# Optimization experiments

Measured on AMD Instinct MI355X. Metric: run time of the kernel, lower is better.

## Reference

```python
import jax, jax.numpy as jnp
import numpy as np

B, L, D_IN = 32, 200, 64
H = 64          # hidden_size
A = 36          # attention_size
NEG_SLOPE = 0.01  # torch LeakyReLU default


def setup_inputs() -> dict:
    key = jax.random.key(0)
    ks = jax.random.split(key, 7)
    s_ln = 1.0 / np.sqrt(D_IN)
    s_w1 = 1.0 / np.sqrt(3 * H)
    s_w2 = 1.0 / np.sqrt(A)
    return {
        "x": jax.random.normal(ks[0], (B, L, D_IN), dtype=jnp.float32),
        "ln_w": jax.random.uniform(ks[1], (D_IN, H), minval=-s_ln, maxval=s_ln, dtype=jnp.float32),
        "ln_b": jax.random.uniform(ks[2], (H,), minval=-s_ln, maxval=s_ln, dtype=jnp.float32),
        "w1": jax.random.uniform(ks[3], (3 * H, A), minval=-s_w1, maxval=s_w1, dtype=jnp.float32),
        "b1": jax.random.uniform(ks[4], (A,), minval=-s_w1, maxval=s_w1, dtype=jnp.float32),
        "w2": jax.random.uniform(ks[5], (A,), minval=-s_w2, maxval=s_w2, dtype=jnp.float32),
        "b2": jax.random.uniform(ks[6], (), minval=-s_w2, maxval=s_w2, dtype=jnp.float32),
    }


def reference(x, ln_w, ln_b, w1, b1, w2, b2):
    # x: [B, L, D_in] -> h: [B, L, H]
    h = jnp.einsum("bld,dh->blh", x, ln_w) + ln_b
    Ld = h.shape[1]
    Hd = h.shape[-1]
    # The torch code concatenates (x1, x2, x1*x2) where x1[b,i,j]=h[b,j],
    # x2[b,i,j]=h[b,i]. Split w1 accordingly instead of materializing the
    # [B,L,L,3H] concat tensor.
    w1a, w1b, w1c = w1[:Hd], w1[Hd:2 * Hd], w1[2 * Hd:]
    a = jnp.einsum("bjh,ha->bja", h, w1a)          # x1 contribution (depends on j)
    c = jnp.einsum("bih,ha->bia", h, w1b)          # x2 contribution (depends on i)
    cross = jnp.einsum("bih,bjh,ha->bija", h, h, w1c)  # (x1*x2) contribution
    pre = a[:, None, :, :] + c[:, :, None, :] + cross + b1   # [B,L,L,A]
    act = jax.nn.leaky_relu(pre, negative_slope=NEG_SLOPE)
    score = jnp.einsum("bija,a->bij", act, w2) + b2          # [B,L,L]
    mask = jnp.tril(jnp.ones((Ld, Ld), dtype=score.dtype))   # causal (incl. diag)
    score = score * mask
    return jnp.einsum("bij,bjh->bih", score, h)               # [B,L,H]
```

## Files before the change

kernel.cpp:

```cpp
#include <hip/hip_runtime.h>

#define B 32
#define L 200
#define DIN 64
#define H 64
#define A 36

typedef __attribute__((ext_vector_type(8))) short short8;
typedef __attribute__((ext_vector_type(4))) float floatx4;
typedef __attribute__((ext_vector_type(8))) float floatx8;

static __device__ __forceinline__ short f2bf(float f) {
    union { float f; unsigned u; } v; v.f = f;
    unsigned r = (v.u + 0x7FFF + ((v.u >> 16) & 1)) >> 16;
    return (short)r;
}
static __device__ __forceinline__ float bf2f(short s) {
    union { unsigned u; float f; } v; v.u = ((unsigned)(unsigned short)s) << 16;
    return v.f;
}

__global__ __launch_bounds__(256) void prep_kernel(
    const float* __restrict__ x, const float* __restrict__ ln_w,
    const float* __restrict__ ln_b, const float* __restrict__ w1,
    float* __restrict__ h_out, float* __restrict__ cc_out, short* __restrict__ hb16_out,
    float* __restrict__ w1a_r, float* __restrict__ w1c_r)
{
    int wave = threadIdx.x >> 6;
    int lane = threadIdx.x & 63;
    int bl = __builtin_amdgcn_readfirstlane(blockIdx.x * 4 + wave);
    const float* xr = x + (size_t)bl * DIN;
    float p0 = ln_b[lane], p1 = 0.f;
    #pragma unroll
    for (int d = 0; d < DIN; d += 2) {
        p0 = fmaf(xr[d],     ln_w[d * H + lane],       p0);
        p1 = fmaf(xr[d + 1], ln_w[(d + 1) * H + lane], p1);
    }
    float acc = p0 + p1;
    __shared__ float hrow[4][H];
    hrow[wave][lane] = acc;
    h_out[(size_t)bl * H + lane] = acc;
    int j = bl % L;
    hb16_out[(size_t)bl * H + (lane ^ ((j & 7) << 3))] = f2bf(acc);
    if (lane < A) {
        float s0 = 0.f, s1 = 0.f;
        #pragma unroll
        for (int hh = 0; hh < H; hh += 2) {
            s0 = fmaf(hrow[wave][hh],     w1[(H + hh) * A + lane],     s0);
            s1 = fmaf(hrow[wave][hh + 1], w1[(H + hh + 1) * A + lane], s1);
        }
        cc_out[(size_t)bl * A + lane] = s0 + s1;
    }
    if (blockIdx.x == 0) {
        for (int idx = threadIdx.x; idx < 2 * 3 * 64 * 8; idx += 256) {
            int e = idx & 7, ln = (idx >> 3) & 63, sn = idx >> 9;
            int s = sn / 3, n = sn - 3 * s;
            int k = s * 32 + (ln >> 4) * 8 + e;
            int c = n * 16 + (ln & 15);
            w1a_r[idx] = (c < A) ? w1[k * A + c] : 0.f;
            w1c_r[idx] = (c < A) ? w1[(2 * H + k) * A + c] : 0.f;
        }
    }
}

__global__ __launch_bounds__(256) void score_kernel(
    const float* __restrict__ h, const short* __restrict__ hb16,
    const float* __restrict__ cc, const float* __restrict__ w1a_r,
    const float* __restrict__ w1c_r, const float* __restrict__ b1,
    const float* __restrict__ w2, const float* __restrict__ b2,
    float* __restrict__ out)
{
    int blk = blockIdx.x;
    int b  = blk / 50;
    int bg = blk - b * 50;
    int wave = threadIdx.x >> 6;
    int lane = threadIdx.x & 63;
    int i = __builtin_amdgcn_readfirstlane(bg + 50 * wave);
    int l15 = lane & 15, l4 = lane >> 4;

    __shared__ __align__(16) short tile[208 * 64];
    __shared__ __align__(16) float slds[4][16];

    const short* hb16b = hb16 + (size_t)b * L * H;

    for (int c = wave; c < 26; c += 4) {
        int j = (c < 25) ? (c * 8 + (lane >> 3)) : (L - 1);
        const short* src = hb16b + (size_t)j * H + (lane & 7) * 8;
        __builtin_amdgcn_global_load_lds(
            (const __attribute__((address_space(1))) void*)src,
            (__attribute__((address_space(3))) void*)&tile[c * 512],
            16, 0, 0);
    }

    const float* hi    = h + ((size_t)b * L + i) * H;
    const float* ccrow = cc + ((size_t)b * L + i) * A;
    float b2v = b2[0];
    float w2v[3][4], cbv[3][4];
    #pragma unroll
    for (int n = 0; n < 3; ++n) {
        #pragma unroll
        for (int r = 0; r < 4; ++r) {
            int a = n * 16 + l4 * 4 + r;
            bool av = a < A;
            w2v[n][r] = av ? w2[a] : 0.f;
            cbv[n][r] = av ? (ccrow[a] + b1[a]) : 0.f;
        }
    }
    short8 afrag[2][3];
    #pragma unroll
    for (int s = 0; s < 2; ++s) {
        float hik[8];
        #pragma unroll
        for (int e = 0; e < 8; ++e) hik[e] = hi[s * 32 + l4 * 8 + e];
        #pragma unroll
        for (int n = 0; n < 3; ++n) {
            floatx8 wa = *(const floatx8*)&w1a_r[(((s * 3 + n) * 64) + lane) * 8];
            floatx8 wc = *(const floatx8*)&w1c_r[(((s * 3 + n) * 64) + lane) * 8];
            #pragma unroll
            for (int e = 0; e < 8; ++e)
                afrag[s][n][e] = f2bf(fmaf(hik[e], wc[e], wa[e]));
        }
    }
    __syncthreads();

    float oacc[4] = {0.f, 0.f, 0.f, 0.f};
    int mmax = (i >> 4) + 1;

    for (int m = 0; m < mmax; ++m) {
        int row = m * 16 + l15;
        const short* brow = tile + row * 64;
        int sw = (l15 & 7) << 3;
        short8 bf0 = *(const short8*)(brow + ((l4 * 8) ^ sw));
        short8 bf1 = *(const short8*)(brow + ((32 + l4 * 8) ^ sw));
        floatx4 c0 = {cbv[0][0], cbv[0][1], cbv[0][2], cbv[0][3]};
        floatx4 c1 = {cbv[1][0], cbv[1][1], cbv[1][2], cbv[1][3]};
        floatx4 c2 = {cbv[2][0], cbv[2][1], cbv[2][2], cbv[2][3]};
        c0 = __builtin_amdgcn_mfma_f32_16x16x32_bf16(afrag[0][0], bf0, c0, 0, 0, 0);
        c1 = __builtin_amdgcn_mfma_f32_16x16x32_bf16(afrag[0][1], bf0, c1, 0, 0, 0);
        c2 = __builtin_amdgcn_mfma_f32_16x16x32_bf16(afrag[0][2], bf0, c2, 0, 0, 0);
        c0 = __builtin_amdgcn_mfma_f32_16x16x32_bf16(afrag[1][0], bf1, c0, 0, 0, 0);
        c1 = __builtin_amdgcn_mfma_f32_16x16x32_bf16(afrag[1][1], bf1, c1, 0, 0, 0);
        c2 = __builtin_amdgcn_mfma_f32_16x16x32_bf16(afrag[1][2], bf1, c2, 0, 0, 0);
        float sp = 0.f;
        #pragma unroll
        for (int r = 0; r < 4; ++r) {
            float v0 = c0[r], v1 = c1[r], v2 = c2[r];
            float a0 = fmaf(0.01f, fminf(v0, 0.f), fmaxf(v0, 0.f));
            float a1 = fmaf(0.01f, fminf(v1, 0.f), fmaxf(v1, 0.f));
            float a2 = fmaf(0.01f, fminf(v2, 0.f), fmaxf(v2, 0.f));
            sp = fmaf(a0, w2v[0][r], sp);
            sp = fmaf(a1, w2v[1][r], sp);
            sp = fmaf(a2, w2v[2][r], sp);
        }
        sp += __shfl_xor(sp, 16, 64);
        sp += __shfl_xor(sp, 32, 64);
        float sc = (row <= i) ? sp + b2v : 0.f;
        if (l4 == 0) slds[wave][l15] = sc;
        #pragma unroll
        for (int rb = 0; rb < 4; ++rb) {
            floatx4 sv = *(const floatx4*)&slds[wave][rb * 4];
            #pragma unroll
            for (int q = 0; q < 4; ++q) {
                int j = m * 16 + rb * 4 + q;
                short hbv = tile[j * 64 + (lane ^ ((j & 7) << 3))];
                oacc[q] = fmaf(sv[q], bf2f(hbv), oacc[q]);
            }
        }
    }

    out[((size_t)b * L + i) * H + lane] = (oacc[0] + oacc[1]) + (oacc[2] + oacc[3]);
}

extern "C" void kernel_launch(void* const* d_in, const int* in_sizes, int n_in,
                              void* d_out, int out_size, void* d_ws, size_t ws_size,
                              hipStream_t stream) {
    const float* x    = (const float*)d_in[0];
    const float* ln_w = (const float*)d_in[1];
    const float* ln_b = (const float*)d_in[2];
    const float* w1   = (const float*)d_in[3];
    const float* b1   = (const float*)d_in[4];
    const float* w2   = (const float*)d_in[5];
    const float* b2   = (const float*)d_in[6];
    float* out = (float*)d_out;

    float* h_ws   = (float*)d_ws;
    float* cc_ws  = h_ws + (size_t)B * L * H;
    short* hb16_ws = (short*)(cc_ws + (size_t)B * L * A);
    float* w1a_r  = (float*)(hb16_ws + (size_t)B * L * H);
    float* w1c_r  = w1a_r + 3072;

    prep_kernel<<<(B * L) / 4, 256, 0, stream>>>(x, ln_w, ln_b, w1, h_ws, cc_ws,
                                                 hb16_ws, w1a_r, w1c_r);
    score_kernel<<<B * 50, 256, 0, stream>>>(h_ws, hb16_ws, cc_ws, w1a_r, w1c_r,
                                             b1, w2, b2, out);
}
```

Baseline: 37.76 us.

## Pair rows i and 199-i per wave to balance causal work and share B tiles

Each wave now handles two query rows, i1 and its mirror 199-i1, so every wave does roughly equal triangular work. The two rows share each loaded B fragment and h-tile read, and the grid is halved to 800 blocks. The tile preload is trimmed to the rows the block needs, and launch bounds request 4 blocks per SM. The cost is higher register pressure from doubled afrag and accumulator state, and fewer blocks to fill the GPU.

```diff
diff --git a/kernel.cpp b/kernel.cpp
--- a/kernel.cpp
+++ b/kernel.cpp
@@ -63,7 +63,7 @@
     }
 }
 
-__global__ __launch_bounds__(256) void score_kernel(
+__global__ __launch_bounds__(256, 4) void score_kernel(
     const float* __restrict__ h, const short* __restrict__ hb16,
     const float* __restrict__ cc, const float* __restrict__ w1a_r,
     const float* __restrict__ w1c_r, const float* __restrict__ b1,
@@ -71,20 +71,23 @@
     float* __restrict__ out)
 {
     int blk = blockIdx.x;
-    int b  = blk / 50;
-    int bg = blk - b * 50;
+    int b  = blk / 25;
+    int bg = blk - b * 25;
     int wave = threadIdx.x >> 6;
     int lane = threadIdx.x & 63;
-    int i = __builtin_amdgcn_readfirstlane(bg + 50 * wave);
+    int i1 = __builtin_amdgcn_readfirstlane(bg * 4 + wave);
+    int i2 = 199 - i1;
     int l15 = lane & 15, l4 = lane >> 4;
 
     __shared__ __align__(16) short tile[208 * 64];
-    __shared__ __align__(16) float slds[4][16];
+    __shared__ __align__(16) float slds[4][2][16];
 
     const short* hb16b = hb16 + (size_t)b * L * H;
 
-    for (int c = wave; c < 26; c += 4) {
-        int j = (c < 25) ? (c * 8 + (lane >> 3)) : (L - 1);
+    int i2max = 199 - 4 * bg;
+    int nch = (((i2max | 15) + 1) + 7) >> 3;
+    for (int c = wave; c < nch; c += 4) {
+        int j = c * 8 + (lane >> 3); if (j > L - 1) j = L - 1;
         const short* src = hb16b + (size_t)j * H + (lane & 7) * 8;
         __builtin_amdgcn_global_load_lds(
             (const __attribute__((address_space(1))) void*)src,
@@ -92,83 +95,131 @@
             16, 0, 0);
     }
 
-    const float* hi    = h + ((size_t)b * L + i) * H;
-    const float* ccrow = cc + ((size_t)b * L + i) * A;
     float b2v = b2[0];
-    float w2v[3][4], cbv[3][4];
+    float w2v[3][4];
     #pragma unroll
     for (int n = 0; n < 3; ++n) {
         #pragma unroll
         for (int r = 0; r < 4; ++r) {
             int a = n * 16 + l4 * 4 + r;
-            bool av = a < A;
-            w2v[n][r] = av ? w2[a] : 0.f;
-            cbv[n][r] = av ? (ccrow[a] + b1[a]) : 0.f;
-        }
-    }
-    short8 afrag[2][3];
+            w2v[n][r] = (a < A) ? w2[a] : 0.f;
+        }
+    }
+    float cbv[2][3][4];
+    short8 afrag[2][2][3];
+    int iv[2] = {i1, i2};
     #pragma unroll
-    for (int s = 0; s < 2; ++s) {
-        float hik[8];
-        #pragma unroll
-        for (int e = 0; e < 8; ++e) hik[e] = hi[s * 32 + l4 * 8 + e];
+    for (int ii = 0; ii < 2; ++ii) {
+        const float* hi    = h + ((size_t)b * L + iv[ii]) * H;
+        const float* ccrow = cc + ((size_t)b * L + iv[ii]) * A;
         #pragma unroll
         for (int n = 0; n < 3; ++n) {
-            floatx8 wa = *(const floatx8*)&w1a_r[(((s * 3 + n) * 64) + lane) * 8];
-            floatx8 wc = *(const floatx8*)&w1c_r[(((s * 3 + n) * 64) + lane) * 8];
-            #pragma unroll
-            for (int e = 0; e < 8; ++e)
-                afrag[s][n][e] = f2bf(fmaf(hik[e], wc[e], wa[e]));
+            #pragma unroll
+            for (int r = 0; r < 4; ++r) {
+                int a = n * 16 + l4 * 4 + r;
+                cbv[ii][n][r] = (a < A) ? (ccrow[a] + b1[a]) : 0.f;
+            }
+        }
+        #pragma unroll
+        for (int s = 0; s < 2; ++s) {
+            float hik[8];
+            #pragma unroll
+            for (int e = 0; e < 8; ++e) hik[e] = hi[s * 32 + l4 * 8 + e];
+            #pragma unroll
+            for (int n = 0; n < 3; ++n) {
+                floatx8 wa = *(const floatx8*)&w1a_r[(((s * 3 + n) * 64) + lane) * 8];
+                floatx8 wc = *(const floatx8*)&w1c_r[(((s * 3 + n) * 64) + lane) * 8];
+                #pragma unroll
+                for (int e = 0; e < 8; ++e)
+                    afrag[ii][s][n][e] = f2bf(fmaf(hik[e], wc[e], wa[e]));
+            }
         }
     }
     __syncthreads();
 
-    float oacc[4] = {0.f, 0.f, 0.f, 0.f};
-    int mmax = (i >> 4) + 1;
-
-    for (int m = 0; m < mmax; ++m) {
+    float oacc1[4] = {0.f, 0.f, 0.f, 0.f};
+    float oacc2[4] = {0.f, 0.f, 0.f, 0.f};
+    int mmax1 = (i1 >> 4) + 1;
+    int mmax2 = (i2 >> 4) + 1;
+
+    for (int m = 0; m < mmax2; ++m) {
         int row = m * 16 + l15;
         const short* brow = tile + row * 64;
         int sw = (l15 & 7) << 3;
         short8 bf0 = *(const short8*)(brow + ((l4 * 8) ^ sw));
         short8 bf1 = *(const short8*)(brow + ((32 + l4 * 8) ^ sw));
-        floatx4 c0 = {cbv[0][0], cbv[0][1], cbv[0][2], cbv[0][3]};
-        floatx4 c1 = {cbv[1][0], cbv[1][1], cbv[1][2], cbv[1][3]};
-        floatx4 c2 = {cbv[2][0], cbv[2][1], cbv[2][2], cbv[2][3]};
-        c0 = __builtin_amdgcn_mfma_f32_16x16x32_bf16(afrag[0][0], bf0, c0, 0, 0, 0);
-        c1 = __builtin_amdgcn_mfma_f32_16x16x32_bf16(afrag[0][1], bf0, c1, 0, 0, 0);
-        c2 = __builtin_amdgcn_mfma_f32_16x16x32_bf16(afrag[0][2], bf0, c2, 0, 0, 0);
-        c0 = __builtin_amdgcn_mfma_f32_16x16x32_bf16(afrag[1][0], bf1, c0, 0, 0, 0);
-        c1 = __builtin_amdgcn_mfma_f32_16x16x32_bf16(afrag[1][1], bf1, c1, 0, 0, 0);
-        c2 = __builtin_amdgcn_mfma_f32_16x16x32_bf16(afrag[1][2], bf1, c2, 0, 0, 0);
-        float sp = 0.f;
-        #pragma unroll
-        for (int r = 0; r < 4; ++r) {
-            float v0 = c0[r], v1 = c1[r], v2 = c2[r];
-            float a0 = fmaf(0.01f, fminf(v0, 0.f), fmaxf(v0, 0.f));
-            float a1 = fmaf(0.01f, fminf(v1, 0.f), fmaxf(v1, 0.f));
-            float a2 = fmaf(0.01f, fminf(v2, 0.f), fmaxf(v2, 0.f));
-            sp = fmaf(a0, w2v[0][r], sp);
-            sp = fmaf(a1, w2v[1][r], sp);
-            sp = fmaf(a2, w2v[2][r], sp);
-        }
-        sp += __shfl_xor(sp, 16, 64);
-        sp += __shfl_xor(sp, 32, 64);
-        float sc = (row <= i) ? sp + b2v : 0.f;
-        if (l4 == 0) slds[wave][l15] = sc;
+        bool do1 = (m < mmax1);
+
+        floatx4 d0 = {cbv[1][0][0], cbv[1][0][1], cbv[1][0][2], cbv[1][0][3]};
+        floatx4 d1 = {cbv[1][1][0], cbv[1][1][1], cbv[1][1][2], cbv[1][1][3]};
+        floatx4 d2 = {cbv[1][2][0], cbv[1][2][1], cbv[1][2][2], cbv[1][2][3]};
+        d0 = __builtin_amdgcn_mfma_f32_16x16x32_bf16(afrag[1][0][0], bf0, d0, 0, 0, 0);
+        d1 = __builtin_amdgcn_mfma_f32_16x16x32_bf16(afrag[1][0][1], bf0, d1, 0, 0, 0);
+        d2 = __builtin_amdgcn_mfma_f32_16x16x32_bf16(afrag[1][0][2], bf0, d2, 0, 0, 0);
+        d0 = __builtin_amdgcn_mfma_f32_16x16x32_bf16(afrag[1][1][0], bf1, d0, 0, 0, 0);
+        d1 = __builtin_amdgcn_mfma_f32_16x16x32_bf16(afrag[1][1][1], bf1, d1, 0, 0, 0);
+        d2 = __builtin_amdgcn_mfma_f32_16x16x32_bf16(afrag[1][1][2], bf1, d2, 0, 0, 0);
+        {
+            float sp = 0.f;
+            #pragma unroll
+            for (int r = 0; r < 4; ++r) {
+                float v0 = d0[r], v1 = d1[r], v2 = d2[r];
+                float a0 = fmaf(0.01f, fminf(v0, 0.f), fmaxf(v0, 0.f));
+                float a1 = fmaf(0.01f, fminf(v1, 0.f), fmaxf(v1, 0.f));
+                float a2 = fmaf(0.01f, fminf(v2, 0.f), fmaxf(v2, 0.f));
+                sp = fmaf(a0, w2v[0][r], sp);
+                sp = fmaf(a1, w2v[1][r], sp);
+                sp = fmaf(a2, w2v[2][r], sp);
+            }
+            sp += __shfl_xor(sp, 16, 64);
+            sp += __shfl_xor(sp, 32, 64);
+            float sc = (row <= i2) ? sp + b2v : 0.f;
+            if (l4 == 0) slds[wave][1][l15] = sc;
+        }
+        if (do1) {
+            floatx4 e0 = {cbv[0][0][0], cbv[0][0][1], cbv[0][0][2], cbv[0][0][3]};
+            floatx4 e1 = {cbv[0][1][0], cbv[0][1][1], cbv[0][1][2], cbv[0][1][3]};
+            floatx4 e2 = {cbv[0][2][0], cbv[0][2][1], cbv[0][2][2], cbv[0][2][3]};
+            e0 = __builtin_amdgcn_mfma_f32_16x16x32_bf16(afrag[0][0][0], bf0, e0, 0, 0, 0);
+            e1 = __builtin_amdgcn_mfma_f32_16x16x32_bf16(afrag[0][0][1], bf0, e1, 0, 0, 0);
+            e2 = __builtin_amdgcn_mfma_f32_16x16x32_bf16(afrag[0][0][2], bf0, e2, 0, 0, 0);
+            e0 = __builtin_amdgcn_mfma_f32_16x16x32_bf16(afrag[0][1][0], bf1, e0, 0, 0, 0);
+            e1 = __builtin_amdgcn_mfma_f32_16x16x32_bf16(afrag[0][1][1], bf1, e1, 0, 0, 0);
+            e2 = __builtin_amdgcn_mfma_f32_16x16x32_bf16(afrag[0][1][2], bf1, e2, 0, 0, 0);
+            float sp = 0.f;
+            #pragma unroll
+            for (int r = 0; r < 4; ++r) {
+                float v0 = e0[r], v1 = e1[r], v2 = e2[r];
+                float a0 = fmaf(0.01f, fminf(v0, 0.f), fmaxf(v0, 0.f));
+                float a1 = fmaf(0.01f, fminf(v1, 0.f), fmaxf(v1, 0.f));
+                float a2 = fmaf(0.01f, fminf(v2, 0.f), fmaxf(v2, 0.f));
+                sp = fmaf(a0, w2v[0][r], sp);
+                sp = fmaf(a1, w2v[1][r], sp);
+                sp = fmaf(a2, w2v[2][r], sp);
+            }
+            sp += __shfl_xor(sp, 16, 64);
+            sp += __shfl_xor(sp, 32, 64);
+            float sc = (row <= i1) ? sp + b2v : 0.f;
+            if (l4 == 0) slds[wave][0][l15] = sc;
+        }
+
         #pragma unroll
         for (int rb = 0; rb < 4; ++rb) {
-            floatx4 sv = *(const floatx4*)&slds[wave][rb * 4];
+            floatx4 sv2 = *(const floatx4*)&slds[wave][1][rb * 4];
+            floatx4 sv1;
+            if (do1) sv1 = *(const floatx4*)&slds[wave][0][rb * 4];
             #pragma unroll
             for (int q = 0; q < 4; ++q) {
                 int j = m * 16 + rb * 4 + q;
-                short hbv = tile[j * 64 + (lane ^ ((j & 7) << 3))];
-                oacc[q] = fmaf(sv[q], bf2f(hbv), oacc[q]);
-            }
-        }
-    }
-
-    out[((size_t)b * L + i) * H + lane] = (oacc[0] + oacc[1]) + (oacc[2] + oacc[3]);
+                float hv = bf2f(tile[j * 64 + (lane ^ ((j & 7) << 3))]);
+                oacc2[q] = fmaf(sv2[q], hv, oacc2[q]);
+                if (do1) oacc1[q] = fmaf(sv1[q], hv, oacc1[q]);
+            }
+        }
+    }
+
+    out[((size_t)b * L + i1) * H + lane] = (oacc1[0] + oacc1[1]) + (oacc1[2] + oacc1[3]);
+    out[((size_t)b * L + i2) * H + lane] = (oacc2[0] + oacc2[1]) + (oacc2[2] + oacc2[3]);
 }
 
 extern "C" void kernel_launch(void* const* d_in, const int* in_sizes, int n_in,
@@ -191,6 +242,6 @@
 
     prep_kernel<<<(B * L) / 4, 256, 0, stream>>>(x, ln_w, ln_b, w1, h_ws, cc_ws,
                                                  hb16_ws, w1a_r, w1c_r);
-    score_kernel<<<B * 50, 256, 0, stream>>>(h_ws, hb16_ws, cc_ws, w1a_r, w1c_r,
+    score_kernel<<<B * 25, 256, 0, stream>>>(h_ws, hb16_ws, cc_ws, w1a_r, w1c_r,
                                              b1, w2, b2, out);
 }
```

Result: slower. 71.09 us (+88.3%).
